# Kernel tuning notes

Measured on AMD Instinct MI355X. Metric: run time of the kernel, lower is better.

## Reference

```python
import jax, jax.numpy as jnp
import numpy as np
from jax import lax

B, LATENT, HC, COND_OUT, H, INPUT = 64, 512, 1024, 512, 1024, 389
S, SEQ = 16, 512
NOTES = SEQ // S  # 32 notes per subsequence
NL = 2


def _lstm_cell(x, h, c, Wih, Whh, bih, bhh):
    # PyTorch LSTM cell, gate order i, f, g, o
    g = x @ Wih.T + h @ Whh.T + bih + bhh
    i, f, gg, o = jnp.split(g, 4, axis=-1)
    c_new = jax.nn.sigmoid(f) * c + jax.nn.sigmoid(i) * jnp.tanh(gg)
    h_new = jax.nn.sigmoid(o) * jnp.tanh(c_new)
    return h_new, c_new


def setup_inputs() -> dict:
    key = jax.random.key(0)
    ks = iter(jax.random.split(key, 32))
    s = 0.03  # ~ PyTorch LSTM uniform(-1/sqrt(H), 1/sqrt(H)) scale
    def W(shape):
        return jax.random.normal(next(ks), shape, jnp.float32) * s
    return {
        "latent": jax.random.normal(next(ks), (B, LATENT), jnp.float32),
        "target": jax.random.randint(next(ks), (B, SEQ), 0, INPUT),
        "teacher_forcing": 0,
        "h0_dec": jax.random.normal(next(ks), (S, NL, B, H), jnp.float32),
        "c0_dec": jax.random.normal(next(ks), (S, NL, B, H), jnp.float32),
        # conductor LSTM (2 layers)
        "Wih_c0": W((4 * HC, LATENT)), "Whh_c0": W((4 * HC, HC)),
        "bih_c0": W((4 * HC,)), "bhh_c0": W((4 * HC,)),
        "Wih_c1": W((4 * HC, HC)), "Whh_c1": W((4 * HC, HC)),
        "bih_c1": W((4 * HC,)), "bhh_c1": W((4 * HC,)),
        # conductor output projection
        "Wco": W((COND_OUT, HC)), "bco": W((COND_OUT,)),
        # decoder LSTM (2 layers); input = concat(prev_note, emb) -> INPUT+COND_OUT
        "Wih_d0": W((4 * H, INPUT + COND_OUT)), "Whh_d0": W((4 * H, H)),
        "bih_d0": W((4 * H,)), "bhh_d0": W((4 * H,)),
        "Wih_d1": W((4 * H, H)), "Whh_d1": W((4 * H, H)),
        "bih_d1": W((4 * H,)), "bhh_d1": W((4 * H,)),
        # decoder output projection
        "Wdo": W((INPUT, H)), "bdo": W((INPUT,)),
    }


def reference(latent, target, teacher_forcing, h0_dec, c0_dec,
              Wih_c0, Whh_c0, bih_c0, bhh_c0, Wih_c1, Whh_c1, bih_c1, bhh_c1,
              Wco, bco,
              Wih_d0, Whh_d0, bih_d0, bhh_d0, Wih_d1, Whh_d1, bih_d1, bhh_d1,
              Wdo, bdo):
    # use_teacher_forcing is hard-coded False in the source; target is unused.
    del target, teacher_forcing

    def outer(carry, xs):
        hc, cc, prev = carry          # hc, cc: [2,B,HC]; prev: [B,INPUT]
        hd_init, cd_init = xs         # [2,B,H] random decoder init per subsequence
        h0, c0 = _lstm_cell(latent, hc[0], cc[0], Wih_c0, Whh_c0, bih_c0, bhh_c0)
        h1, c1 = _lstm_cell(h0, hc[1], cc[1], Wih_c1, Whh_c1, bih_c1, bhh_c1)
        emb = jnp.tanh(h1 @ Wco.T + bco)  # [B, COND_OUT]

        def inner(ic, _):
            p, hdi, cdi = ic
            x = jnp.concatenate([p, emb], axis=-1)  # [B, INPUT+COND_OUT]
            hd0, cd0 = _lstm_cell(x, hdi[0], cdi[0], Wih_d0, Whh_d0, bih_d0, bhh_d0)
            hd1, cd1 = _lstm_cell(hd0, hdi[1], cdi[1], Wih_d1, Whh_d1, bih_d1, bhh_d1)
            note = jnp.tanh(hd1 @ Wdo.T + bdo)  # [B, INPUT]
            return (note, jnp.stack([hd0, hd1]), jnp.stack([cd0, cd1])), note

        (prev_new, _, _), notes = lax.scan(inner, (prev, hd_init, cd_init), None, length=NOTES)
        return (jnp.stack([h0, h1]), jnp.stack([c0, c1]), prev_new), notes

    init = (jnp.zeros((NL, B, HC), jnp.float32),
            jnp.zeros((NL, B, HC), jnp.float32),
            jnp.zeros((B, INPUT), jnp.float32))
    _, out = lax.scan(outer, init, (h0_dec, c0_dec))
    # out: [S, NOTES, B, INPUT] -> [B, SEQ, INPUT]
    return out.transpose(2, 0, 1, 3).reshape(B, SEQ, INPUT)
```

## Files before the change

### kernel.cpp

```cpp
#include <hip/hip_runtime.h>
#include <hip/hip_bf16.h>

typedef unsigned int  u32;
typedef unsigned short u16;
typedef __attribute__((ext_vector_type(8))) short short8;
typedef __attribute__((ext_vector_type(4))) float f32x4;
typedef __attribute__((ext_vector_type(4))) unsigned int u32x4;
typedef __attribute__((ext_vector_type(2))) unsigned int u32x2;

#define MFMA(a,b,c) __builtin_amdgcn_mfma_f32_16x16x32_bf16(a,b,c,0,0,0)

#define NWG    256
#define KD0    1448
#define KD1    2056
#define KPROJ  1032

#define WS_ARR   0
#define WS_DONE  1024
#define WS_SEM   1536
#define SEM_HD0  0
#define SEM_HD1  1
#define SEM_NOTE 2
#define SEM_I0   3
#define SEM_I1   4

#define WS_NOTE  4096
#define WS_HD0   (WS_NOTE + 2*52*64*8*2)
#define WS_HD1   (WS_HD0 + 2*128*64*8*2)
#define WS_HC0   (WS_HD1 + 2*128*64*8*2)
#define WS_HC1   (WS_HC0 + 2*128*64*8*2)
#define WS_EMB   (WS_HC1 + 2*128*64*8*2)
#define WS_LAT   (WS_EMB + 15*64*64*8*2)
#define WS_END   (WS_EMB + 16*64*64*8*2)

#define NOTE_PAR 26624
#define HD_PAR   65536
#define HC_PAR   65536
#define EMB_S    32768

#define L_GSC   0
#define L_GC0X  8448
#define L_CC0   12800
#define L_CC1   13824
#define L_BC1   14848
#define L_PACK  14912
#define L_ROLE  16960
#define L_WD0   L_ROLE
#define L_G0E   (L_ROLE + 32*KD0*2)
#define L_CST0  (L_G0E + 8448)
#define L_BD0   (L_CST0 + 2048)
#define L_WPJ   (L_BD0 + 128)
#define L_BPJ   (L_WPJ + 16*KPROJ*2)
#define L_WD1   L_ROLE
#define L_CST1  (L_ROLE + 32*KD1*2)
#define L_BD1   (L_CST1 + 2048)
#define LDS_BYTES 153600

__device__ __forceinline__ u16 f2bf(float f){
  u32 u = __float_as_uint(f);
  u32 r = (u + 0x7FFFu + ((u >> 16) & 1u)) >> 16;
  return (u16)r;
}
__device__ __forceinline__ float sigm(float x){ return 1.f/(1.f + __expf(-x)); }
__device__ __forceinline__ float tanh_(float x){
  float e = __expf(-2.f*fabsf(x));
  float t = (1.f - e)/(1.f + e);
  return x < 0.f ? -t : t;
}
__device__ __forceinline__ short8 ldw8(const float* p0){
  short8 r;
#pragma unroll
  for (int j = 0; j < 8; ++j) r[j] = (short)f2bf(p0[j]);
  return r;
}

__device__ __forceinline__ void gst1(u32* p, u32 v){
  asm volatile("global_store_dword %0, %1, off sc1" :: "v"(p), "v"(v) : "memory");
}
__device__ __forceinline__ void gst4(u16* p, u32x4 v){
  asm volatile("global_store_dwordx4 %0, %1, off sc1" :: "v"(p), "v"(v) : "memory");
}
__device__ __forceinline__ u32 ld1_sc1(const u32* p){
  u32 v;
  asm volatile("global_load_dword %0, %1, off sc1\n\ts_waitcnt vmcnt(0)"
               : "=v"(v) : "v"(p) : "memory");
  return v;
}

#define AISSUE(dst, addr) \
  asm volatile("global_load_dwordx4 %0, %1, off sc1" : "=&v"(dst) : "v"(addr) : "memory")
#define AWAITN(cnt) do{ \
  asm volatile("s_waitcnt vmcnt(" #cnt ")" ::: "memory"); \
  __builtin_amdgcn_sched_barrier(0x3F7); }while(0)

template<int NA, int NB, bool TWO>
__device__ __forceinline__ void mm_lds(
    const u16* Wl, int ldw16, const u16* xal, const u16* xbl,
    f32x4& a0, f32x4& a1)
{
  constexpr int N = NA + NB;
  short8 ab[(N < 16) ? N : 16];
#define XADDR(i) (((i) < NA) ? (xal + (size_t)(i)*2048) : (xbl + (size_t)((i)-NA)*2048))
#define ACONS(i) { \
    a0 = MFMA(ab[(i)&15], *(const short8*)(Wl + (size_t)(i)*32), a0); \
    if constexpr (TWO) a1 = MFMA(ab[(i)&15], *(const short8*)(Wl + ldw16 + (size_t)(i)*32), a1); }
  if constexpr (N <= 16){
#pragma unroll
    for (int i = 0; i < N; ++i) AISSUE(ab[i], XADDR(i));
    AWAITN(0);
#pragma unroll
    for (int i = 0; i < N; ++i) ACONS(i);
  } else {
#pragma unroll
    for (int i = 0; i < 16; ++i) AISSUE(ab[i], XADDR(i));
#pragma unroll
    for (int i = 0; i < N - 16; ++i){
      AWAITN(15);
      ACONS(i);
      AISSUE(ab[i & 15], XADDR(i + 16));
    }
#define ATAIL(j, c) AWAITN(c); ACONS(N - 16 + (j));
    ATAIL(0,15) ATAIL(1,14) ATAIL(2,13) ATAIL(3,12)
    ATAIL(4,11) ATAIL(5,10) ATAIL(6,9)  ATAIL(7,8)
    ATAIL(8,7)  ATAIL(9,6)  ATAIL(10,5) ATAIL(11,4)
    ATAIL(12,3) ATAIL(13,2) ATAIL(14,1) ATAIL(15,0)
#undef ATAIL
  }
#undef ACONS
#undef XADDR
}

template<int NA, int NB, bool TWO>
__device__ __forceinline__ void mm_gw(
    const float* w00, const float* w01, const float* w10, const float* w11,
    const u16* xal, const u16* xbl, f32x4& a0, f32x4& a1)
{
  constexpr int N = NA + NB;
  static_assert((N % 16) == 0, "");
  short8 ab[16];
#define XADDR(i) (((i) < NA) ? (xal + (size_t)(i)*2048) : (xbl + (size_t)((i)-NA)*2048))
#pragma unroll
  for (int b = 0; b < N/16; ++b){
#pragma unroll
    for (int j = 0; j < 16; ++j) AISSUE(ab[j], XADDR(b*16 + j));
    AWAITN(0);
#pragma unroll
    for (int j = 0; j < 16; ++j){
      const int i = b*16 + j;
      const float* wp0 = (i < NA) ? (w00 + (size_t)i*32) : (w01 + (size_t)(i-NA)*32);
      a0 = MFMA(ab[j], ldw8(wp0), a0);
      if constexpr (TWO){
        const float* wp1 = (i < NA) ? (w10 + (size_t)i*32) : (w11 + (size_t)(i-NA)*32);
        a1 = MFMA(ab[j], ldw8(wp1), a1);
      }
    }
  }
#undef XADDR
}

__device__ __forceinline__ void sem_post(char* ws, int sem, int wg){
  asm volatile("s_waitcnt vmcnt(0)" ::: "memory");
  __syncthreads();
  if (threadIdx.x == 0){
    u32* c = (u32*)(ws + WS_SEM + sem*512 + (wg & 7)*64);
    __hip_atomic_fetch_add(c, 1u, __ATOMIC_RELAXED, __HIP_MEMORY_SCOPE_AGENT);
  }
}
__device__ __forceinline__ void sem_wait(char* ws, int sem, u32 target, bool slp){
  if (threadIdx.x < 64){
    const int l = threadIdx.x;
    const u32* c = (const u32*)(ws + WS_SEM + sem*512 + l*64);
    for (;;){
      u32 v = (l < 8) ? ld1_sc1(c) : 0u;
#pragma unroll
      for (int off = 32; off; off >>= 1)
        v += (u32)__shfl_xor((int)v, off, 64);
      if (v >= target) break;
      if (slp) __builtin_amdgcn_s_sleep(1);
    }
  }
  __syncthreads();
}

__device__ __forceinline__ void gbar(char* ws, int grp, int mem, u32 ep){
  u32* arr  = (u32*)(ws + WS_ARR) + grp*32;
  u32* done = (u32*)(ws + WS_DONE);
  asm volatile("s_waitcnt vmcnt(0)" ::: "memory");
  __syncthreads();
  if (threadIdx.x < 64){
    const int l = threadIdx.x;
    if (l == 0) gst1(&arr[mem], ep);
    if (mem == 0){
      for (;;){
        u32 m = (l < 32) ? ld1_sc1(&arr[l]) : ep;
#pragma unroll
        for (int off = 32; off; off >>= 1){
          u32 o = (u32)__shfl_xor((int)m, off, 64);
          m = o < m ? o : m;
        }
        if (m >= ep) break;
      }
      if (l == 0) gst1(&done[grp], ep);
    }
    for (;;){
      u32 m = (l < 8) ? ld1_sc1(&done[l]) : ep;
#pragma unroll
      for (int off = 32; off; off >>= 1){
        u32 o = (u32)__shfl_xor((int)m, off, 64);
        m = o < m ? o : m;
      }
      if (m >= ep) break;
      __builtin_amdgcn_s_sleep(1);
    }
  }
  __syncthreads();
}

struct Params {
  const float *latent, *h0_dec, *c0_dec;
  const float *Wih_c0, *Whh_c0, *bih_c0, *bhh_c0;
  const float *Wih_c1, *Whh_c1, *bih_c1, *bhh_c1;
  const float *Wco, *bco;
  const float *Wih_d0, *Whh_d0, *bih_d0, *bhh_d0;
  const float *Wih_d1, *Whh_d1, *bih_d1, *bhh_d1;
  const float *Wdo, *bdo;
  float* out;
  char* ws;
};

__device__ __forceinline__ void cell_pw(
    const float* g_sc, const float* gadd, const float* bias,
    float* cst, u32* pack, int tid)
{
  const int b = tid & 63, k = tid >> 6;
  u32 hp = 0;
#pragma unroll
  for (int j = 0; j < 2; ++j){
    const int u = 2*k + j;
    float gi = g_sc[b*33 + u];
    float gf = g_sc[b*33 + 8 + u];
    float gg = g_sc[b*33 + 16 + u];
    float go = g_sc[b*33 + 24 + u];
    if (gadd){
      gi += gadd[b*33 + u];      gf += gadd[b*33 + 8 + u];
      gg += gadd[b*33 + 16 + u]; go += gadd[b*33 + 24 + u];
    }
    if (bias){
      gi += bias[u]; gf += bias[8 + u]; gg += bias[16 + u]; go += bias[24 + u];
    }
    float c = sigm(gf)*cst[u*64 + b] + sigm(gi)*tanh_(gg);
    const float h = sigm(go)*tanh_(c);
    cst[u*64 + b] = c;
    hp |= ((u32)f2bf(h)) << (16*j);
  }
  pack[b*4 + k] = hp;
}

__device__ __forceinline__ void cond_pw(
    f32x4 acc, const float* gadd17, const float* bias16,
    float* cstL, u16* pack16, int lane, int wid)
{
  const int r = lane & 15, q = lane >> 4, m0 = wid*16;
  float v[4], vf[4], vg[4], vo[4];
#pragma unroll
  for (int i = 0; i < 4; ++i){
    const int brow = m0 + q*4 + i;
    float x = acc[i];
    if (gadd17) x += gadd17[brow*17 + r];
    if (bias16) x += bias16[r];
    v[i] = x;
  }
#pragma unroll
  for (int i = 0; i < 4; ++i){
    vf[i] = __shfl_xor(v[i], 4, 64);
    vg[i] = __shfl_xor(v[i], 8, 64);
    vo[i] = __shfl_xor(v[i], 12, 64);
  }
  if (r < 4){
#pragma unroll
    for (int i = 0; i < 4; ++i){
      const int brow = m0 + q*4 + i;
      float c = sigm(vf[i])*cstL[r*64 + brow] + sigm(v[i])*tanh_(vg[i]);
      const float h = sigm(vo[i])*tanh_(c);
      cstL[r*64 + brow] = c;
      pack16[brow*4 + r] = f2bf(h);
    }
  }
}

__global__ void init_kernel(const float* latent, char* ws){
  const int i = blockIdx.x*blockDim.x + threadIdx.x;
  if (i < 1024) ((u32*)ws)[i] = 0u;
  if (i < 26624) ((u32*)(ws + WS_NOTE))[i] = 0u;
  if (i < 65536){ ((u32*)(ws + WS_HC0))[i] = 0u; ((u32*)(ws + WS_HC1))[i] = 0u; }
  if (i < 32768){
    const int b = i >> 9, k = i & 511;
    ((u16*)(ws + WS_LAT))[((size_t)(k >> 3)*64 + b)*8 + (k & 7)] = f2bf(latent[i]);
  }
}

__global__ void __launch_bounds__(256, 1) decoder_kernel(Params P){
  extern __shared__ char smem[];
  const int wg = blockIdx.x, tid = threadIdx.x;
  const int lane = tid & 63, wid = tid >> 6;
  const int rr = lane & 15, q = lane >> 4, m0 = wid*16;
  const int grp = wg >> 5, mem = wg & 31;

  u16* noteb = (u16*)(P.ws + WS_NOTE);
  u16* hd0b  = (u16*)(P.ws + WS_HD0);
  u16* hd1b  = (u16*)(P.ws + WS_HD1);
  u16* hc0b  = (u16*)(P.ws + WS_HC0);
  u16* hc1b  = (u16*)(P.ws + WS_HC1);
  u16* embA  = (u16*)(P.ws + WS_EMB);
  const u16* latg = (const u16*)(P.ws + WS_LAT);

  float* g_sc  = (float*)(smem + L_GSC);
  float* g_c0x = (float*)(smem + L_GC0X);
  float* cc0   = (float*)(smem + L_CC0);
  float* cc1   = (float*)(smem + L_CC1);
  float* bc1   = (float*)(smem + L_BC1);
  u16*   pack16 = (u16*)(smem + L_PACK);
  u32*   packU32 = (u32*)(smem + L_PACK);
  u16*   Wd0  = (u16*)(smem + L_WD0);
  float* g0e  = (float*)(smem + L_G0E);
  float* cst0 = (float*)(smem + L_CST0);
  float* bd0  = (float*)(smem + L_BD0);
  u16*   Wpj  = (u16*)(smem + L_WPJ);
  float* bpj  = (float*)(smem + L_BPJ);
  u16*   Wd1  = (u16*)(smem + L_WD1);
  float* cst1 = (float*)(smem + L_CST1);
  float* bd1  = (float*)(smem + L_BD1);

  const bool is_d0 = (wg < 128);
  const int lofs = (q*64 + m0 + rr)*8;

  if (is_d0){
    for (int r = wid; r < 32; r += 4){
      const int grow = ((r >> 3) << 10) + 8*wg + (r & 7);
      const float* wih = P.Wih_d0 + (size_t)grow*901;
      const float* whh = P.Whh_d0 + (size_t)grow*1024;
      u16* dst = Wd0 + (size_t)r*KD0;
      for (int c = lane; c < 416; c += 64) dst[c] = (c < 389) ? f2bf(wih[c]) : (u16)0;
      for (int c = lane; c < 1024; c += 64) dst[416 + c] = f2bf(whh[c]);
    }
    if (tid < 32){
      const int grow = ((tid >> 3) << 10) + 8*wg + (tid & 7);
      bd0[tid] = P.bih_d0[grow] + P.bhh_d0[grow];
    }
    if (wg < 25){
      for (int r = wid; r < 16; r += 4){
        const int row = 16*wg + r;
        u16* dst = Wpj + (size_t)r*KPROJ;
        if (row < 389){
          const float* w = P.Wdo + (size_t)row*1024;
          for (int c = lane; c < 1024; c += 64) dst[c] = f2bf(w[c]);
        } else {
          for (int c = lane; c < 1024; c += 64) dst[c] = 0;
        }
      }
      if (tid < 16){
        const int row = 16*wg + tid;
        bpj[tid] = (row < 389) ? P.bdo[row] : 0.f;
      }
    }
  } else {
    const int wl = wg - 128;
    for (int r = wid; r < 32; r += 4){
      const int grow = ((r >> 3) << 10) + 8*wl + (r & 7);
      const float* wih = P.Wih_d1 + (size_t)grow*1024;
      const float* whh = P.Whh_d1 + (size_t)grow*1024;
      u16* dst = Wd1 + (size_t)r*KD1;
      for (int c = lane; c < 1024; c += 64) dst[c] = f2bf(wih[c]);
      for (int c = lane; c < 1024; c += 64) dst[1024 + c] = f2bf(whh[c]);
    }
    if (tid < 32){
      const int grow = ((tid >> 3) << 10) + 8*wl + (tid & 7);
      bd1[tid] = P.bih_d1[grow] + P.bhh_d1[grow];
    }
  }
  if (tid < 256){ cc0[tid] = 0.f; cc1[tid] = 0.f; }
  if (tid < 16){
    const int grow = ((tid >> 2) << 10) + 4*wg + (tid & 3);
    bc1[tid] = P.bih_c1[grow] + P.bhh_c1[grow];
  }
  {
    const int grow = ((rr >> 2) << 10) + 4*wg + (rr & 3);
    f32x4 acc = {0.f,0.f,0.f,0.f}, dummy;
    mm_gw<16,0,false>(P.Wih_c0 + (size_t)grow*512 + q*8, nullptr, nullptr, nullptr,
                      latg + lofs, latg + lofs, acc, dummy);
    const float bias = P.bih_c0[grow] + P.bhh_c0[grow];
#pragma unroll
    for (int i = 0; i < 4; ++i)
      g_c0x[(m0 + q*4 + i)*17 + rr] = acc[i] + bias;
  }
  __syncthreads();

  u32 ep = 0;
#define GBAR() gbar(P.ws, grp, mem, ++ep)

  for (int s = 0; s < 16; ++s){
    const int pc = s & 1;
    const u16* hc0_p = hc0b + (size_t)pc*HC_PAR;
    u16*       hc0_n = hc0b + (size_t)(pc ^ 1)*HC_PAR;
    const u16* hc1_p = hc1b + (size_t)pc*HC_PAR;
    u16*       hc1_n = hc1b + (size_t)(pc ^ 1)*HC_PAR;
    const int grow = ((rr >> 2) << 10) + 4*wg + (rr & 3);

    {
      f32x4 acc = {0.f,0.f,0.f,0.f}, dummy;
      mm_gw<32,0,false>(P.Whh_c0 + (size_t)grow*1024 + q*8, nullptr, nullptr, nullptr,
                        hc0_p + lofs, hc0_p + lofs, acc, dummy);
      cond_pw(acc, g_c0x, nullptr, cc0, pack16, lane, wid);
    }
    __syncthreads();
    if (tid < 64){
      u32x2 v = *(const u32x2*)&packU32[tid*2];
      asm volatile("global_store_dwordx2 %0, %1, off sc1"
                   :: "v"(hc0_n + ((size_t)(wg >> 1)*64 + tid)*8 + (wg & 1)*4), "v"(v) : "memory");
    }
    GBAR();

    {
      f32x4 acc = {0.f,0.f,0.f,0.f}, dummy;
      mm_gw<32,32,false>(P.Wih_c1 + (size_t)grow*1024 + q*8,
                         P.Whh_c1 + (size_t)grow*1024 + q*8, nullptr, nullptr,
                         hc0_n + lofs, hc1_p + lofs, acc, dummy);
      cond_pw(acc, nullptr, bc1, cc1, pack16, lane, wid);
    }
    __syncthreads();
    if (tid < 64){
      u32x2 v = *(const u32x2*)&packU32[tid*2];
      asm volatile("global_store_dwordx2 %0, %1, off sc1"
                   :: "v"(hc1_n + ((size_t)(wg >> 1)*64 + tid)*8 + (wg & 1)*4), "v"(v) : "memory");
    }
    GBAR();

    if (wg < 32){
      const int row = 16*wg + rr;
      f32x4 acc = {0.f,0.f,0.f,0.f}, dummy;
      mm_gw<32,0,false>(P.Wco + (size_t)row*1024 + q*8, nullptr, nullptr, nullptr,
                        hc1_n + lofs, hc1_n + lofs, acc, dummy);
      const float bias = P.bco[row];
#pragma unroll
      for (int i = 0; i < 4; ++i)
        pack16[(m0 + q*4 + i)*16 + rr] = f2bf(tanh_(acc[i] + bias));
      __syncthreads();
      if (tid < 64){
        u16* ea = embA + (size_t)s*EMB_S;
        u32x4 v0 = *(const u32x4*)&packU32[tid*8];
        u32x4 v1 = *(const u32x4*)&packU32[tid*8 + 4];
        gst4(ea + ((size_t)(2*wg)*64 + tid)*8, v0);
        gst4(ea + ((size_t)(2*wg + 1)*64 + tid)*8, v1);
      }
    }
    GBAR();
  }

  for (int s = 0; s < 16; ++s){
    const u32 n0 = (u32)s*32u;
    f32x4 sh0 = {0.f,0.f,0.f,0.f}, sh1 = sh0;
    f32x4 t10 = sh0, t11 = sh0;

    sem_wait(P.ws, SEM_NOTE, 25u*n0, true);

    if (is_d0){
      {
        const int b = tid & 63, k = tid >> 6;
        const size_t src = ((size_t)(s*2 + 0)*64 + b)*1024 + 8*wg + 2*k;
        cst0[(2*k)*64 + b]     = P.c0_dec[src];
        cst0[(2*k + 1)*64 + b] = P.c0_dec[src + 1];
        packU32[b*4 + k] = (u32)f2bf(P.h0_dec[src]) | ((u32)f2bf(P.h0_dec[src + 1]) << 16);
      }
      __syncthreads();
      if (tid < 64){
        u32x4 v = *(const u32x4*)&packU32[tid*4];
        gst4(hd0b + ((size_t)wg*64 + tid)*8, v);
      }
      sem_post(P.ws, SEM_I0, wg);
      {
        const int g0 = ((rr >> 3) << 10) + 8*wg + (rr & 7);
        const int g1 = (((rr + 16) >> 3) << 10) + 8*wg + (rr & 7);
        f32x4 a0 = {0.f,0.f,0.f,0.f}, a1 = {0.f,0.f,0.f,0.f};
        const u16* ea = embA + (size_t)s*EMB_S;
        mm_gw<16,0,true>(P.Wih_d0 + (size_t)g0*901 + 389 + q*8, nullptr,
                         P.Wih_d0 + (size_t)g1*901 + 389 + q*8, nullptr,
                         ea + lofs, ea + lofs, a0, a1);
#pragma unroll
        for (int i = 0; i < 4; ++i){
          g0e[(m0 + q*4 + i)*33 + rr]      = a0[i] + bd0[rr];
          g0e[(m0 + q*4 + i)*33 + 16 + rr] = a1[i] + bd0[rr + 16];
        }
      }
      __syncthreads();
    } else {
      const int wl = wg - 128;
      const int b = tid & 63, k = tid >> 6;
      const size_t src = ((size_t)(s*2 + 1)*64 + b)*1024 + 8*wl + 2*k;
      cst1[(2*k)*64 + b]     = P.c0_dec[src];
      cst1[(2*k + 1)*64 + b] = P.c0_dec[src + 1];
      packU32[b*4 + k] = (u32)f2bf(P.h0_dec[src]) | ((u32)f2bf(P.h0_dec[src + 1]) << 16);
      __syncthreads();
      if (tid < 64){
        u32x4 v = *(const u32x4*)&packU32[tid*4];
        gst4(hd1b + ((size_t)wl*64 + tid)*8, v);
      }
      sem_post(P.ws, SEM_I1, wg);
    }

    for (int t = 0; t < 32; ++t){
      const u32 n = n0 + (u32)t;
      const int p = t & 1;
      const u16* note_p = noteb + (size_t)p*NOTE_PAR;
      u16*       note_n = noteb + (size_t)(p ^ 1)*NOTE_PAR;
      const u16* hd0_p = hd0b + (size_t)p*HD_PAR;
      u16*       hd0_n = hd0b + (size_t)(p ^ 1)*HD_PAR;
      const u16* hd1_p = hd1b + (size_t)p*HD_PAR;
      u16*       hd1_n = hd1b + (size_t)(p ^ 1)*HD_PAR;

      if (is_d0){
        if (t == 0) sem_wait(P.ws, SEM_I0, 128u*(u32)(s + 1), false);
        else        sem_wait(P.ws, SEM_NOTE, 25u*n, false);

        f32x4 a0, a1;
        if (t == 0){
          a0 = (f32x4){0.f,0.f,0.f,0.f}; a1 = a0;
          mm_lds<13,32,true>(Wd0 + (size_t)rr*KD0 + q*8, 16*KD0,
                             note_p + lofs, hd0_p + lofs, a0, a1);
        } else {
          a0 = sh0; a1 = sh1;
          mm_lds<13,0,true>(Wd0 + (size_t)rr*KD0 + q*8, 16*KD0,
                            note_p + lofs, note_p + lofs, a0, a1);
        }
#pragma unroll
        for (int i = 0; i < 4; ++i){
          g_sc[(m0 + q*4 + i)*33 + rr]      = a0[i];
          g_sc[(m0 + q*4 + i)*33 + 16 + rr] = a1[i];
        }
        __syncthreads();
        cell_pw(g_sc, g0e, nullptr, cst0, packU32, tid);
        __syncthreads();
        if (tid < 64){
          u32x4 v = *(const u32x4*)&packU32[tid*4];
          gst4(hd0_n + ((size_t)wg*64 + tid)*8, v);
        }
        sem_post(P.ws, SEM_HD0, wg);

        if (t < 31){
          sem_wait(P.ws, SEM_HD0, 128u*(n + 1u), false);
          sh0 = (f32x4){0.f,0.f,0.f,0.f}; sh1 = sh0;
          mm_lds<32,0,true>(Wd0 + (size_t)rr*KD0 + 416 + q*8, 16*KD0,
                            hd0_n + lofs, hd0_n + lofs, sh0, sh1);
        }

        if (wg < 25){
          sem_wait(P.ws, SEM_HD1, 128u*(n + 1u), false);
          f32x4 b0 = {0.f,0.f,0.f,0.f}, b1;
          mm_lds<32,0,false>(Wpj + (size_t)rr*KPROJ + q*8, 0,
                             hd1_n + lofs, hd1_n + lofs, b0, b1);
          const int row = 16*wg + rr;
          const int seq = s*32 + t;
          const float bias = bpj[rr];
#pragma unroll
          for (int i = 0; i < 4; ++i){
            const int brow = m0 + q*4 + i;
            const float nv = tanh_(b0[i] + bias);
            if (row < 389) P.out[((size_t)brow*512 + seq)*389 + row] = nv;
            pack16[brow*16 + rr] = f2bf(nv);
          }
          __syncthreads();
          if (tid < 64){
            u32x4 v0 = *(const u32x4*)&packU32[tid*8];
            u32x4 v1 = *(const u32x4*)&packU32[tid*8 + 4];
            gst4(note_n + ((size_t)(2*wg)*64 + tid)*8, v0);
            gst4(note_n + ((size_t)(2*wg + 1)*64 + tid)*8, v1);
          }
          sem_post(P.ws, SEM_NOTE, wg);
        }
      } else {
        sem_wait(P.ws, SEM_HD0, 128u*(n + 1u), false);
        if (t == 0) sem_wait(P.ws, SEM_I1, 128u*(u32)(s + 1), false);

        f32x4 a0, a1;
        if (t == 0){
          a0 = (f32x4){0.f,0.f,0.f,0.f}; a1 = a0;
          mm_lds<32,32,true>(Wd1 + (size_t)rr*KD1 + q*8, 16*KD1,
                             hd0_n + lofs, hd1_p + lofs, a0, a1);
        } else {
          a0 = t10; a1 = t11;
          mm_lds<32,0,true>(Wd1 + (size_t)rr*KD1 + q*8, 16*KD1,
                            hd0_n + lofs, hd0_n + lofs, a0, a1);
        }
#pragma unroll
        for (int i = 0; i < 4; ++i){
          g_sc[(m0 + q*4 + i)*33 + rr]      = a0[i];
          g_sc[(m0 + q*4 + i)*33 + 16 + rr] = a1[i];
        }
        __syncthreads();
        cell_pw(g_sc, nullptr, bd1, cst1, packU32, tid);
        __syncthreads();
        if (tid < 64){
          u32x4 v = *(const u32x4*)&packU32[tid*4];
          gst4(hd1_n + ((size_t)(wg - 128)*64 + tid)*8, v);
        }
        sem_post(P.ws, SEM_HD1, wg);

        if (t < 31){
          sem_wait(P.ws, SEM_HD1, 128u*(n + 1u), false);
          t10 = (f32x4){0.f,0.f,0.f,0.f}; t11 = t10;
          mm_lds<32,0,true>(Wd1 + (size_t)rr*KD1 + 1024 + q*8, 16*KD1,
                            hd1_n + lofs, hd1_n + lofs, t10, t11);
        }
      }
    }
  }
#undef GBAR
}

extern "C" void kernel_launch(void* const* d_in, const int* in_sizes, int n_in,
                              void* d_out, int out_size, void* d_ws, size_t ws_size,
                              hipStream_t stream){
  (void)in_sizes; (void)n_in; (void)out_size;
  if (ws_size < (size_t)WS_END) return;

  Params P;
  P.latent = (const float*)d_in[0];
  P.h0_dec = (const float*)d_in[3];
  P.c0_dec = (const float*)d_in[4];
  P.Wih_c0 = (const float*)d_in[5];  P.Whh_c0 = (const float*)d_in[6];
  P.bih_c0 = (const float*)d_in[7];  P.bhh_c0 = (const float*)d_in[8];
  P.Wih_c1 = (const float*)d_in[9];  P.Whh_c1 = (const float*)d_in[10];
  P.bih_c1 = (const float*)d_in[11]; P.bhh_c1 = (const float*)d_in[12];
  P.Wco    = (const float*)d_in[13]; P.bco    = (const float*)d_in[14];
  P.Wih_d0 = (const float*)d_in[15]; P.Whh_d0 = (const float*)d_in[16];
  P.bih_d0 = (const float*)d_in[17]; P.bhh_d0 = (const float*)d_in[18];
  P.Wih_d1 = (const float*)d_in[19]; P.Whh_d1 = (const float*)d_in[20];
  P.bih_d1 = (const float*)d_in[21]; P.bhh_d1 = (const float*)d_in[22];
  P.Wdo    = (const float*)d_in[23]; P.bdo    = (const float*)d_in[24];
  P.out = (float*)d_out;
  P.ws  = (char*)d_ws;

  hipLaunchKernelGGL(init_kernel, dim3(256), dim3(256), 0, stream,
                     (const float*)d_in[0], (char*)d_ws);

  hipFuncSetAttribute(reinterpret_cast<const void*>(&decoder_kernel),
                      hipFuncAttributeMaxDynamicSharedMemorySize, LDS_BYTES);
  hipLaunchKernelGGL(decoder_kernel, dim3(NWG), dim3(256), LDS_BYTES, stream, P);
}
```

Before: 9.346 ms.

## Deepen activation prefetch to 32 loads and lighten semaphore post/wait

```diff
diff --git a/kernel.cpp b/kernel.cpp
--- a/kernel.cpp
+++ b/kernel.cpp
@@ -99,12 +99,13 @@
     f32x4& a0, f32x4& a1)
 {
   constexpr int N = NA + NB;
-  short8 ab[(N < 16) ? N : 16];
+  constexpr int R = (N < 32) ? N : 32;
+  short8 ab[R];
 #define XADDR(i) (((i) < NA) ? (xal + (size_t)(i)*2048) : (xbl + (size_t)((i)-NA)*2048))
 #define ACONS(i) { \
-    a0 = MFMA(ab[(i)&15], *(const short8*)(Wl + (size_t)(i)*32), a0); \
-    if constexpr (TWO) a1 = MFMA(ab[(i)&15], *(const short8*)(Wl + ldw16 + (size_t)(i)*32), a1); }
-  if constexpr (N <= 16){
+    a0 = MFMA(ab[(i) % R], *(const short8*)(Wl + (size_t)(i)*32), a0); \
+    if constexpr (TWO) a1 = MFMA(ab[(i) % R], *(const short8*)(Wl + ldw16 + (size_t)(i)*32), a1); }
+  if constexpr (N <= 32){
 #pragma unroll
     for (int i = 0; i < N; ++i) AISSUE(ab[i], XADDR(i));
     AWAITN(0);
@@ -112,19 +113,16 @@
     for (int i = 0; i < N; ++i) ACONS(i);
   } else {
 #pragma unroll
-    for (int i = 0; i < 16; ++i) AISSUE(ab[i], XADDR(i));
-#pragma unroll
-    for (int i = 0; i < N - 16; ++i){
-      AWAITN(15);
+    for (int i = 0; i < 32; ++i) AISSUE(ab[i], XADDR(i));
+#pragma unroll
+    for (int i = 0; i < N - 32; ++i){
+      AWAITN(31);
       ACONS(i);
-      AISSUE(ab[i & 15], XADDR(i + 16));
-    }
-#define ATAIL(j, c) AWAITN(c); ACONS(N - 16 + (j));
-    ATAIL(0,15) ATAIL(1,14) ATAIL(2,13) ATAIL(3,12)
-    ATAIL(4,11) ATAIL(5,10) ATAIL(6,9)  ATAIL(7,8)
-    ATAIL(8,7)  ATAIL(9,6)  ATAIL(10,5) ATAIL(11,4)
-    ATAIL(12,3) ATAIL(13,2) ATAIL(14,1) ATAIL(15,0)
-#undef ATAIL
+      AISSUE(ab[i & 31], XADDR(i + 32));
+    }
+    AWAITN(0);
+#pragma unroll
+    for (int i = N - 32; i < N; ++i) ACONS(i);
   }
 #undef ACONS
 #undef XADDR
@@ -158,15 +156,14 @@
 #undef XADDR
 }
 
-__device__ __forceinline__ void sem_post(char* ws, int sem, int wg){
+__device__ __forceinline__ void sem_post_lane(char* ws, int sem, int wg){
   asm volatile("s_waitcnt vmcnt(0)" ::: "memory");
-  __syncthreads();
   if (threadIdx.x == 0){
     u32* c = (u32*)(ws + WS_SEM + sem*512 + (wg & 7)*64);
     __hip_atomic_fetch_add(c, 1u, __ATOMIC_RELAXED, __HIP_MEMORY_SCOPE_AGENT);
   }
 }
-__device__ __forceinline__ void sem_wait(char* ws, int sem, u32 target, bool slp){
+__device__ __forceinline__ void sem_wait(char* ws, int sem, u32 target){
   if (threadIdx.x < 64){
     const int l = threadIdx.x;
     const u32* c = (const u32*)(ws + WS_SEM + sem*512 + l*64);
@@ -176,7 +173,7 @@
       for (int off = 32; off; off >>= 1)
         v += (u32)__shfl_xor((int)v, off, 64);
       if (v >= target) break;
-      if (slp) __builtin_amdgcn_s_sleep(1);
+      __builtin_amdgcn_s_sleep(1);
     }
   }
   __syncthreads();
@@ -461,7 +458,7 @@
     f32x4 sh0 = {0.f,0.f,0.f,0.f}, sh1 = sh0;
     f32x4 t10 = sh0, t11 = sh0;
 
-    sem_wait(P.ws, SEM_NOTE, 25u*n0, true);
+    sem_wait(P.ws, SEM_NOTE, 25u*n0);
 
     if (is_d0){
       {
@@ -475,8 +472,8 @@
       if (tid < 64){
         u32x4 v = *(const u32x4*)&packU32[tid*4];
         gst4(hd0b + ((size_t)wg*64 + tid)*8, v);
-      }
-      sem_post(P.ws, SEM_I0, wg);
+        sem_post_lane(P.ws, SEM_I0, wg);
+      }
       {
         const int g0 = ((rr >> 3) << 10) + 8*wg + (rr & 7);
         const int g1 = (((rr + 16) >> 3) << 10) + 8*wg + (rr & 7);
@@ -503,8 +500,8 @@
       if (tid < 64){
         u32x4 v = *(const u32x4*)&packU32[tid*4];
         gst4(hd1b + ((size_t)wl*64 + tid)*8, v);
-      }
-      sem_post(P.ws, SEM_I1, wg);
+        sem_post_lane(P.ws, SEM_I1, wg);
+      }
     }
 
     for (int t = 0; t < 32; ++t){
@@ -518,8 +515,8 @@
       u16*       hd1_n = hd1b + (size_t)(p ^ 1)*HD_PAR;
 
       if (is_d0){
-        if (t == 0) sem_wait(P.ws, SEM_I0, 128u*(u32)(s + 1), false);
-        else        sem_wait(P.ws, SEM_NOTE, 25u*n, false);
+        if (t == 0) sem_wait(P.ws, SEM_I0, 128u*(u32)(s + 1));
+        else        sem_wait(P.ws, SEM_NOTE, 25u*n);
 
         f32x4 a0, a1;
         if (t == 0){
@@ -542,18 +539,18 @@
         if (tid < 64){
           u32x4 v = *(const u32x4*)&packU32[tid*4];
           gst4(hd0_n + ((size_t)wg*64 + tid)*8, v);
-        }
-        sem_post(P.ws, SEM_HD0, wg);
+          sem_post_lane(P.ws, SEM_HD0, wg);
+        }
 
         if (t < 31){
-          sem_wait(P.ws, SEM_HD0, 128u*(n + 1u), false);
+          sem_wait(P.ws, SEM_HD0, 128u*(n + 1u));
           sh0 = (f32x4){0.f,0.f,0.f,0.f}; sh1 = sh0;
           mm_lds<32,0,true>(Wd0 + (size_t)rr*KD0 + 416 + q*8, 16*KD0,
                             hd0_n + lofs, hd0_n + lofs, sh0, sh1);
         }
 
         if (wg < 25){
-          sem_wait(P.ws, SEM_HD1, 128u*(n + 1u), false);
+          sem_wait(P.ws, SEM_HD1, 128u*(n + 1u));
           f32x4 b0 = {0.f,0.f,0.f,0.f}, b1;
           mm_lds<32,0,false>(Wpj + (size_t)rr*KPROJ + q*8, 0,
                              hd1_n + lofs, hd1_n + lofs, b0, b1);
@@ -573,12 +570,12 @@
             u32x4 v1 = *(const u32x4*)&packU32[tid*8 + 4];
             gst4(note_n + ((size_t)(2*wg)*64 + tid)*8, v0);
             gst4(note_n + ((size_t)(2*wg + 1)*64 + tid)*8, v1);
+            sem_post_lane(P.ws, SEM_NOTE, wg);
           }
-          sem_post(P.ws, SEM_NOTE, wg);
         }
       } else {
-        sem_wait(P.ws, SEM_HD0, 128u*(n + 1u), false);
-        if (t == 0) sem_wait(P.ws, SEM_I1, 128u*(u32)(s + 1), false);
+        sem_wait(P.ws, SEM_HD0, 128u*(n + 1u));
+        if (t == 0) sem_wait(P.ws, SEM_I1, 128u*(u32)(s + 1));
 
         f32x4 a0, a1;
         if (t == 0){
@@ -601,11 +598,11 @@
         if (tid < 64){
           u32x4 v = *(const u32x4*)&packU32[tid*4];
           gst4(hd1_n + ((size_t)(wg - 128)*64 + tid)*8, v);
-        }
-        sem_post(P.ws, SEM_HD1, wg);
+          sem_post_lane(P.ws, SEM_HD1, wg);
+        }
 
         if (t < 31){
-          sem_wait(P.ws, SEM_HD1, 128u*(n + 1u), false);
+          sem_wait(P.ws, SEM_HD1, 128u*(n + 1u));
           t10 = (f32x4){0.f,0.f,0.f,0.f}; t11 = t10;
           mm_lds<32,0,true>(Wd1 + (size_t)rr*KD1 + 1024 + q*8, 16*KD1,
                             hd1_n + lofs, hd1_n + lofs, t10, t11);
```

Result: slower. 9.752 ms (+4.4%).
